# Kernel tuning notes

Hardware: AMD Instinct MI355X
Metric: run time of the kernel (lower is better)

## Reference

```python
import jax, jax.numpy as jnp
import numpy as np

N_NODES = 100000
N_EDGES = 1600000
FEAT_DIM = 64
IN_DIM = FEAT_DIM + 3  # feat + xyz


def setup_inputs() -> dict:
    key = jax.random.key(0)
    k1, k2, k3, k4, k5 = jax.random.split(key, 5)
    xyz = jax.random.normal(k1, (N_NODES, 3), dtype=jnp.float32)
    feat = jax.random.normal(k2, (N_NODES, FEAT_DIM), dtype=jnp.float32)
    edge_index = jax.random.randint(k3, (2, N_EDGES), 0, N_NODES, dtype=jnp.int64)
    # MLP params (Linear stored as [in, out] for x @ W + b)
    W1 = jax.random.normal(k4, (2 * IN_DIM, FEAT_DIM), dtype=jnp.float32) * (1.0 / np.sqrt(2 * IN_DIM))
    b1 = jnp.zeros((FEAT_DIM,), dtype=jnp.float32)
    W2 = jax.random.normal(k5, (FEAT_DIM, FEAT_DIM), dtype=jnp.float32) * (1.0 / np.sqrt(FEAT_DIM))
    b2 = jnp.zeros((FEAT_DIM,), dtype=jnp.float32)
    return {"xyz": xyz, "feat": feat, "edge_index": edge_index,
            "W1": W1, "b1": b1, "W2": W2, "b2": b2}


def reference(xyz, feat, edge_index, W1, b1, W2, b2):
    # node features: cat([feat, xyz]) -> [N, C+3]
    x = jnp.concatenate([feat, xyz], axis=-1)
    src = edge_index[0]  # j (source / neighbor)
    dst = edge_index[1]  # i (target, aggregation index)
    x_i = x[dst]                       # [E, C+3]
    x_j = x[src]                       # [E, C+3]
    # EdgeConv message: mlp(cat([x_i, x_j - x_i]))
    m = jnp.concatenate([x_i, x_j - x_i], axis=-1)   # [E, 2*(C+3)]
    h = jax.nn.relu(m @ W1 + b1) @ W2 + b2           # [E, C]
    n = x.shape[0]
    agg = jax.ops.segment_max(h, dst, num_segments=n)  # [N, C]
    # nodes with no incoming edges get 0 (matches PyG scatter-max fill)
    deg = jax.ops.segment_sum(jnp.ones((dst.shape[0],), h.dtype), dst, num_segments=n)
    return jnp.where(deg[:, None] > 0, agg, jnp.zeros_like(agg))
```

## Files before the change

kernel.cpp:

```cpp
#include <hip/hip_runtime.h>
#include <stdint.h>

#define N_NODES 100000
#define FEAT 64
#define NB 64
#define SC_CHUNK 8192
#define NBKT 1563
#define BKT_CAP 1400
#define RVN 6
#define BIAS 512.0f
#define NT_NODES 64
#define XT_STRIDE 68
#define SMEM_BYTES (67 * XT_STRIDE * 4 + 2 * 67 * 64 * 4)

typedef __attribute__((ext_vector_type(8))) _Float16 half8;
typedef __attribute__((ext_vector_type(2))) _Float16 half2v;
typedef __attribute__((ext_vector_type(2))) __fp16 fp16x2;
typedef __attribute__((ext_vector_type(4))) float f32x4;

__device__ __forceinline__ uint32_t enc_key(float f) {
    uint32_t u = __float_as_uint(f);
    return (u & 0x80000000u) ? ~u : (u | 0x80000000u);
}
__device__ __forceinline__ float dec_key(uint32_t k) {
    return __uint_as_float((k & 0x80000000u) ? (k & 0x7FFFFFFFu) : ~k);
}
__device__ __forceinline__ uint32_t pk_f16(float a, float b) {
    union { fp16x2 h; uint32_t u; } cv;
    cv.h = __builtin_amdgcn_cvt_pkrtz(a, b);
    return cv.u;
}

#define W2T_OFF 0
#define AMB_OFF 4096
#define BM_OFF  8384
#define W2P_OFF 12672
#define U_OFF   16384
#define V_OFF   (U_OFF + N_NODES * FEAT / 2)
#define GCNT_OFF (U_OFF + N_NODES * FEAT)
#define SRT_OFF  (GCNT_OFF + 2048)

__global__ __launch_bounds__(256) void transform_kernel(
    const float* __restrict__ W1, const float* __restrict__ W2,
    float* __restrict__ ws, int full)
{
    int i = blockIdx.x * 256 + threadIdx.x;
    if (i < 4096) {
        int c2 = i >> 6, c = i & 63;
        ws[W2T_OFF + i] = W2[c * 64 + c2];
    }
}

__global__ __launch_bounds__(256) void nodebkt_kernel(
    const float* __restrict__ xyz, const float* __restrict__ feat,
    const float* __restrict__ b1, const float* __restrict__ W1,
    const float* __restrict__ W2, float* __restrict__ ws,
    uint16_t* __restrict__ U, uint16_t* __restrict__ V, int nN,
    const int* __restrict__ ei, uint32_t* __restrict__ gcnt,
    uint32_t* __restrict__ sorted, int nE, int nBkt, int nodeBlocks)
{
    extern __shared__ float smem[];
    int t = threadIdx.x;

    if ((int)blockIdx.x < nBkt) {
        uint32_t* hist = (uint32_t*)smem;
        int e0 = blockIdx.x * SC_CHUNK;
        int cnt = min(SC_CHUNK, nE - e0);
        int cnt4 = cnt & ~3;

        for (int i = t; i < NBKT; i += 256) hist[i] = 0;
        __syncthreads();
        for (int i = t * 4; i < cnt4; i += 1024) {
            uint4 d4 = *(const uint4*)(ei + nE + e0 + i);
            atomicAdd(&hist[d4.x >> 6], 1u);
            atomicAdd(&hist[d4.y >> 6], 1u);
            atomicAdd(&hist[d4.z >> 6], 1u);
            atomicAdd(&hist[d4.w >> 6], 1u);
        }
        for (int i = cnt4 + t; i < cnt; i += 256)
            atomicAdd(&hist[ei[nE + e0 + i] >> 6], 1u);
        __syncthreads();
        for (int b = t; b < NBKT; b += 256) {
            uint32_t c = hist[b];
            hist[b] = c ? atomicAdd(&gcnt[b], c) : 0u;
        }
        __syncthreads();
        for (int i = t * 4; i < cnt4; i += 1024) {
            uint4 s4 = *(const uint4*)(ei + e0 + i);
            uint4 d4 = *(const uint4*)(ei + nE + e0 + i);
            uint32_t sa[4] = {(uint32_t)s4.x, (uint32_t)s4.y, (uint32_t)s4.z, (uint32_t)s4.w};
            uint32_t da[4] = {(uint32_t)d4.x, (uint32_t)d4.y, (uint32_t)d4.z, (uint32_t)d4.w};
            #pragma unroll
            for (int k = 0; k < 4; ++k) {
                uint32_t b = da[k] >> 6;
                uint32_t pos = atomicAdd(&hist[b], 1u);
                if (pos < BKT_CAP)
                    sorted[(size_t)b * BKT_CAP + pos] = sa[k] | ((da[k] & 63u) << 20);
            }
        }
        for (int i = cnt4 + t; i < cnt; i += 256) {
            uint32_t src = (uint32_t)ei[e0 + i];
            uint32_t dst = (uint32_t)ei[nE + e0 + i];
            uint32_t b = dst >> 6;
            uint32_t pos = atomicAdd(&hist[b], 1u);
            if (pos < BKT_CAP)
                sorted[(size_t)b * BKT_CAP + pos] = src | ((dst & 63u) << 20);
        }
        return;
    }

    int nb = (int)blockIdx.x - nBkt;
    if (nb >= nodeBlocks) {
        int p = (nb - nodeBlocks) * 256 + t;
        if (p < 4096) {
            int j = p & 7, c2lo = (p >> 3) & 15, quad = (p >> 7) & 3;
            int h = (p >> 9) & 1, n4 = (p >> 10) & 3;
            int k = h * 32 + quad * 8 + j;
            int n = n4 * 16 + c2lo;
            ((_Float16*)(ws + W2P_OFF))[p] = (_Float16)W2[k * 64 + n];
        }
        return;
    }

    float* xt = smem;
    float* wA = smem + 67 * XT_STRIDE;
    float* wB = wA + 67 * 64;

    int nb0 = nb * NT_NODES;
    int rows = min(NT_NODES, nN - nb0);

    for (int i4 = t; i4 < 67 * 16; i4 += 256) {
        float4 a = *(const float4*)(W1 + i4 * 4);
        float4 b = *(const float4*)(W1 + 67 * 64 + i4 * 4);
        float4 d;
        d.x = a.x - b.x; d.y = a.y - b.y; d.z = a.z - b.z; d.w = a.w - b.w;
        *(float4*)(wA + i4 * 4) = d;
        *(float4*)(wB + i4 * 4) = b;
    }
    for (int g4 = t; g4 < rows * 16; g4 += 256) {
        int row = g4 >> 4, c4 = (g4 & 15) * 4;
        float4 v = *(const float4*)(feat + (size_t)(nb0 + row) * FEAT + c4);
        xt[(c4 + 0) * XT_STRIDE + row] = v.x;
        xt[(c4 + 1) * XT_STRIDE + row] = v.y;
        xt[(c4 + 2) * XT_STRIDE + row] = v.z;
        xt[(c4 + 3) * XT_STRIDE + row] = v.w;
    }
    for (int i = t; i < 3 * NT_NODES; i += 256) {
        int k3 = i >> 6, row = i & 63;
        float v = (row < rows) ? xyz[(size_t)(nb0 + row) * 3 + k3] : 0.0f;
        xt[(64 + k3) * XT_STRIDE + row] = v;
    }
    __syncthreads();

    int cb = (t & 15) * 4;
    int ng = (t >> 4) * 4;

    float accU[4][4], accV[4][4];
    #pragma unroll
    for (int c = 0; c < 4; ++c) {
        float bv = b1[cb + c];
        #pragma unroll
        for (int r = 0; r < 4; ++r) { accU[r][c] = bv; accV[r][c] = 0.0f; }
    }

    const float* xrow = xt + ng;
    #pragma unroll 2
    for (int k = 0; k < 67; ++k) {
        float4 x0 = *(const float4*)(xrow + k * XT_STRIDE);
        float4 wa = *(const float4*)(wA + k * 64 + cb);
        float4 wb = *(const float4*)(wB + k * 64 + cb);
        float xv[4] = {x0.x, x0.y, x0.z, x0.w};
        float wav[4] = {wa.x, wa.y, wa.z, wa.w};
        float wbv[4] = {wb.x, wb.y, wb.z, wb.w};
        #pragma unroll
        for (int r = 0; r < 4; ++r) {
            #pragma unroll
            for (int c = 0; c < 4; ++c) {
                accU[r][c] = fmaf(xv[r], wav[c], accU[r][c]);
                accV[r][c] = fmaf(xv[r], wbv[c], accV[r][c]);
            }
        }
    }

    #pragma unroll
    for (int r = 0; r < 4; ++r) {
        if (ng + r < rows) {
            size_t n = (size_t)(nb0 + ng + r);
            uint2 oU; oU.x = pk_f16(accU[r][0], accU[r][1]);
                      oU.y = pk_f16(accU[r][2], accU[r][3]);
            *(uint2*)(U + n * FEAT + cb) = oU;
            uint2 oV; oV.x = pk_f16(accV[r][0], accV[r][1]);
                      oV.y = pk_f16(accV[r][2], accV[r][3]);
            *(uint2*)(V + n * FEAT + cb) = oV;
        }
    }
}

#define LOADE(G, DSV, VV0, VV1, UU0, UU1) do {                               \
        int e_c_ = min((G) + el, cnt - 1);                                   \
        uint32_t val_ = ssrt[e_c_];                                          \
        DSV = *(const uint4*)(ssrt + (G) + quad * 4);                        \
        int src_ = (int)(val_ & 0xFFFFFu);                                   \
        const uint32_t* vr_ = (const uint32_t*)(V + (size_t)src_ * FEAT);    \
        VV0 = *(const uint4*)(vr_ + quad * 4);                               \
        VV1 = *(const uint4*)(vr_ + 16 + quad * 4);                          \
        const uint32_t* ur_ = ushare + (int)(val_ >> 20) * 32;               \
        UU0 = *(const uint4*)(ur_ + quad * 4);                               \
        UU1 = *(const uint4*)(ur_ + 16 + quad * 4);                          \
    } while (0)

__global__ __launch_bounds__(256) void agg_kernel(
    const uint32_t* __restrict__ gcnt, const uint32_t* __restrict__ sorted,
    const uint16_t* __restrict__ U, const uint16_t* __restrict__ V,
    const float* __restrict__ ws_w2p, const float* __restrict__ b2,
    float* __restrict__ out, int nN)
{
    __shared__ int      lmax[NB * 65];
    __shared__ uint32_t ushare[NB * 32];
    __shared__ uint32_t ssrt[BKT_CAP + 16];
    __shared__ uint32_t shist[NB];

    int bkt = blockIdx.x;
    int nb0 = bkt * NB;
    int rows = min(NB, nN - nb0);
    int cnt = min((int)gcnt[bkt], BKT_CAP);
    int t = threadIdx.x;

    for (int i = t; i < NB * 65; i += 256) lmax[i] = 0;
    if (t < NB) shist[t] = 0;
    {
        const uint4* usrc4 = (const uint4*)(U + (size_t)nb0 * FEAT);
        for (int i = t; i < rows * 8; i += 256) ((uint4*)ushare)[i] = usrc4[i];
    }
    const uint32_t* bsrc = sorted + (size_t)bkt * BKT_CAP;
    __syncthreads();

    uint32_t rv[RVN];
    #pragma unroll
    for (int j = 0; j < RVN; ++j) {
        int i = t + j * 256;
        if (i < cnt) {
            uint32_t v = bsrc[i];
            rv[j] = v;
            atomicAdd(&shist[v >> 20], 1u);
        }
    }
    __syncthreads();
    if (t < NB) {
        uint32_t v = shist[t];
        uint32_t run = v;
        #pragma unroll
        for (int d = 1; d < 64; d <<= 1) {
            uint32_t x = (uint32_t)__shfl_up((int)run, (unsigned)d, 64);
            if (t >= d) run += x;
        }
        shist[t] = run - v;
    }
    __syncthreads();
    #pragma unroll
    for (int j = 0; j < RVN; ++j) {
        int i = t + j * 256;
        if (i < cnt) {
            uint32_t v = rv[j];
            uint32_t pos = atomicAdd(&shist[v >> 20], 1u);
            ssrt[pos] = v;
        }
    }
    __syncthreads();

    int lane = t & 63;
    int wave = t >> 6;
    int el = lane & 15, quad = lane >> 4;

    const uint4* w2p = (const uint4*)ws_w2p;
    union { uint4 u4; half8 h8; } bfr[8];
    #pragma unroll
    for (int q8 = 0; q8 < 8; ++q8)
        bfr[q8].u4 = w2p[(q8 * 4 + quad) * 16 + el];
    float b2v[4];
    #pragma unroll
    for (int n4 = 0; n4 < 4; ++n4) b2v[n4] = b2[n4 * 16 + el] + BIAS;

    const half2v zero2 = {(_Float16)0.0f, (_Float16)0.0f};

    uint4 dsv_c, vv_c0, vv_c1, uu_c0, uu_c1;
    int g = wave * 16;
    if (g < cnt) LOADE(g, dsv_c, vv_c0, vv_c1, uu_c0, uu_c1);

    #pragma unroll 1
    for (; g < cnt; g += 64) {
        int gn = g + 64;
        int gl = (gn < cnt) ? gn : g;
        uint4 dsv_n, vv_n0, vv_n1, uu_n0, uu_n1;
        LOADE(gl, dsv_n, vv_n0, vv_n1, uu_n0, uu_n1);

        union { uint4 u4; half8 h8; } afr[2];
        #pragma unroll
        for (int h = 0; h < 2; ++h) {
            uint4 uu = h ? uu_c1 : uu_c0;
            uint4 vv = h ? vv_c1 : vv_c0;
            uint32_t ua[4] = {uu.x, uu.y, uu.z, uu.w};
            uint32_t va[4] = {vv.x, vv.y, vv.z, vv.w};
            uint32_t pk[4];
            #pragma unroll
            for (int p = 0; p < 4; ++p) {
                union { uint32_t u; half2v h2; } cu, cv2, ct;
                cu.u = ua[p]; cv2.u = va[p];
                ct.h2 = __builtin_elementwise_max(cu.h2 + cv2.h2, zero2);
                pk[p] = ct.u;
            }
            afr[h].u4 = make_uint4(pk[0], pk[1], pk[2], pk[3]);
        }

        f32x4 acc[4];
        #pragma unroll
        for (int n4 = 0; n4 < 4; ++n4)
            acc[n4] = (f32x4){b2v[n4], b2v[n4], b2v[n4], b2v[n4]};
        #pragma unroll
        for (int n4 = 0; n4 < 4; ++n4) {
            acc[n4] = __builtin_amdgcn_mfma_f32_16x16x32_f16(afr[0].h8, bfr[n4*2+0].h8, acc[n4], 0, 0, 0);
            acc[n4] = __builtin_amdgcn_mfma_f32_16x16x32_f16(afr[1].h8, bfr[n4*2+1].h8, acc[n4], 0, 0, 0);
        }

        int d0 = (int)(dsv_c.x >> 20), d1 = (int)(dsv_c.y >> 20);
        int d2 = (int)(dsv_c.z >> 20), d3 = (int)(dsv_c.w >> 20);
        int eb = g + quad * 4;
        bool ok0 = eb < cnt, ok1 = eb + 1 < cnt;
        bool ok2 = eb + 2 < cnt, ok3 = eb + 3 < cnt;
        bool m0 = (d0 == d1) & ok1;
        bool m1 = (d1 == d2) & ok2;
        bool m2 = (d2 == d3) & ok3;
        #pragma unroll
        for (int n4 = 0; n4 < 4; ++n4) {
            if (m0) acc[n4][1] = fmaxf(acc[n4][1], acc[n4][0]);
            if (m1) acc[n4][2] = fmaxf(acc[n4][2], acc[n4][1]);
            if (m2) acc[n4][3] = fmaxf(acc[n4][3], acc[n4][2]);
        }
        if (ok0 & !m0) {
            #pragma unroll
            for (int n4 = 0; n4 < 4; ++n4)
                atomicMax(&lmax[d0 * 65 + n4 * 16 + el], __float_as_int(acc[n4][0]));
        }
        if (ok1 & !m1) {
            #pragma unroll
            for (int n4 = 0; n4 < 4; ++n4)
                atomicMax(&lmax[d1 * 65 + n4 * 16 + el], __float_as_int(acc[n4][1]));
        }
        if (ok2 & !m2) {
            #pragma unroll
            for (int n4 = 0; n4 < 4; ++n4)
                atomicMax(&lmax[d2 * 65 + n4 * 16 + el], __float_as_int(acc[n4][2]));
        }
        if (ok3) {
            #pragma unroll
            for (int n4 = 0; n4 < 4; ++n4)
                atomicMax(&lmax[d3 * 65 + n4 * 16 + el], __float_as_int(acc[n4][3]));
        }

        dsv_c = dsv_n;
        vv_c0 = vv_n0; vv_c1 = vv_n1;
        uu_c0 = uu_n0; uu_c1 = uu_n1;
    }
    __syncthreads();

    for (int i = t * 4; i < rows * FEAT; i += 1024) {
        int r = i >> 6, c = i & 63;
        int lb = r * 65 + c;
        int k0 = lmax[lb + 0], k1 = lmax[lb + 1];
        int k2 = lmax[lb + 2], k3 = lmax[lb + 3];
        float4 o;
        o.x = k0 ? (__int_as_float(k0) - BIAS) : 0.0f;
        o.y = k1 ? (__int_as_float(k1) - BIAS) : 0.0f;
        o.z = k2 ? (__int_as_float(k2) - BIAS) : 0.0f;
        o.w = k3 ? (__int_as_float(k3) - BIAS) : 0.0f;
        *(float4*)(out + (size_t)(nb0 + r) * FEAT + c) = o;
    }
}
#undef LOADE

__device__ __forceinline__ void rank1_update(
    float* __restrict__ h, float xi, float d,
    const float* __restrict__ A, const float* __restrict__ B)
{
    #pragma unroll
    for (int c = 0; c < FEAT; ++c)
        h[c] = fmaf(xi, A[c], fmaf(d, B[c], h[c]));
}

__global__ __launch_bounds__(256) void edge_fused_kernel(
    const float* __restrict__ xyz, const float* __restrict__ feat,
    const int* __restrict__ ei,
    const float* __restrict__ W1, const float* __restrict__ b1,
    const float* __restrict__ ws, const float* __restrict__ b2,
    uint32_t* __restrict__ keys, int nE)
{
    int e = blockIdx.x * 256 + threadIdx.x;
    if (e >= nE) return;
    int src = ei[e];
    int dst = ei[nE + e];
    const float* __restrict__ W2T = ws + W2T_OFF;

    float h[FEAT];
    #pragma unroll
    for (int c = 0; c < FEAT; ++c) h[c] = b1[c];

    const float* fi = feat + (size_t)dst * FEAT;
    const float* fj = feat + (size_t)src * FEAT;
    #pragma unroll 1
    for (int k = 0; k < 64; k += 4) {
        float4 a = *(const float4*)(fi + k);
        float4 b = *(const float4*)(fj + k);
        rank1_update(h, a.x, b.x - a.x, W1 + (k + 0) * 64, W1 + (67 + k + 0) * 64);
        rank1_update(h, a.y, b.y - a.y, W1 + (k + 1) * 64, W1 + (67 + k + 1) * 64);
        rank1_update(h, a.z, b.z - a.z, W1 + (k + 2) * 64, W1 + (67 + k + 2) * 64);
        rank1_update(h, a.w, b.w - a.w, W1 + (k + 3) * 64, W1 + (67 + k + 3) * 64);
    }
    {
        const float* pi = xyz + (size_t)dst * 3;
        const float* pj = xyz + (size_t)src * 3;
        #pragma unroll
        for (int k3 = 0; k3 < 3; ++k3) {
            float xi = pi[k3];
            rank1_update(h, xi, pj[k3] - xi, W1 + (64 + k3) * 64, W1 + (131 + k3) * 64);
        }
    }
    #pragma unroll
    for (int c = 0; c < FEAT; ++c) h[c] = fmaxf(h[c], 0.0f);

    uint32_t* krow = keys + (size_t)dst * FEAT;
    #pragma unroll 1
    for (int c2 = 0; c2 < FEAT; c2 += 4) {
        float o0 = b2[c2 + 0], o1 = b2[c2 + 1];
        float o2 = b2[c2 + 2], o3 = b2[c2 + 3];
        const float* w0 = W2T + (c2 + 0) * 64;
        const float* w1 = W2T + (c2 + 1) * 64;
        const float* w2 = W2T + (c2 + 2) * 64;
        const float* w3 = W2T + (c2 + 3) * 64;
        #pragma unroll
        for (int c = 0; c < FEAT; ++c) {
            float hv = h[c];
            o0 = fmaf(hv, w0[c], o0);
            o1 = fmaf(hv, w1[c], o1);
            o2 = fmaf(hv, w2[c], o2);
            o3 = fmaf(hv, w3[c], o3);
        }
        uint32_t k0 = enc_key(o0), k1 = enc_key(o1);
        uint32_t k2 = enc_key(o2), k3 = enc_key(o3);
        uint4 cur = *(const uint4*)(krow + c2);
        if (k0 > cur.x) atomicMax(&krow[c2 + 0], k0);
        if (k1 > cur.y) atomicMax(&krow[c2 + 1], k1);
        if (k2 > cur.z) atomicMax(&krow[c2 + 2], k2);
        if (k3 > cur.w) atomicMax(&krow[c2 + 3], k3);
    }
}

__global__ __launch_bounds__(256) void decode_kernel(
    uint32_t* __restrict__ keys, int n4)
{
    int i = blockIdx.x * 256 + threadIdx.x;
    if (i >= n4) return;
    uint4 k = ((const uint4*)keys)[i];
    float4 r;
    r.x = k.x ? dec_key(k.x) : 0.0f;
    r.y = k.y ? dec_key(k.y) : 0.0f;
    r.z = k.z ? dec_key(k.z) : 0.0f;
    r.w = k.w ? dec_key(k.w) : 0.0f;
    ((float4*)keys)[i] = r;
}

extern "C" void kernel_launch(void* const* d_in, const int* in_sizes, int n_in,
                              void* d_out, int out_size, void* d_ws, size_t ws_size,
                              hipStream_t stream)
{
    const float* xyz  = (const float*)d_in[0];
    const float* feat = (const float*)d_in[1];
    const int*   ei   = (const int*)d_in[2];
    const float* W1   = (const float*)d_in[3];
    const float* b1   = (const float*)d_in[4];
    const float* W2   = (const float*)d_in[5];
    const float* b2   = (const float*)d_in[6];

    int nE = in_sizes[2] / 2;
    float* ws = (float*)d_ws;

    size_t need_words = (size_t)SRT_OFF + (size_t)NBKT * BKT_CAP;
    int full = (ws_size >= need_words * 4) ? 1 : 0;

    if (full) {
        uint16_t* U = (uint16_t*)(ws + U_OFF);
        uint16_t* V = (uint16_t*)(ws + V_OFF);
        uint32_t* gcnt   = (uint32_t*)(ws + GCNT_OFF);
        uint32_t* sorted = (uint32_t*)(ws + SRT_OFF);

        hipMemsetAsync(gcnt, 0, NBKT * sizeof(uint32_t), stream);
        int nBkt = (nE + SC_CHUNK - 1) / SC_CHUNK;
        int nodeBlocks = (N_NODES + NT_NODES - 1) / NT_NODES;
        int packBlocks = 16;
        nodebkt_kernel<<<nBkt + nodeBlocks + packBlocks, 256, SMEM_BYTES, stream>>>(
            xyz, feat, b1, W1, W2, ws, U, V, N_NODES, ei, gcnt, sorted, nE,
            nBkt, nodeBlocks);
        agg_kernel<<<NBKT, 256, 0, stream>>>(
            gcnt, sorted, U, V, ws + W2P_OFF, b2, (float*)d_out, N_NODES);
    } else {
        uint32_t* keys = (uint32_t*)d_out;
        transform_kernel<<<16, 256, 0, stream>>>(W1, W2, ws, 0);
        hipMemsetAsync(d_out, 0, (size_t)out_size * sizeof(float), stream);
        edge_fused_kernel<<<(nE + 255) / 256, 256, 0, stream>>>(
            xyz, feat, ei, W1, b1, ws, b2, keys, nE);
        decode_kernel<<<(out_size / 4 + 255) / 256, 256, 0, stream>>>(
            keys, out_size / 4);
    }
}
```

Before: 173.5 us.

## Fold edge bucketing into node blocks via global atomics; pad shared U rows

Removes the separate bucket-scatter blocks, which built a shared-memory histogram and reserved ranges per chunk. Instead, each node-transform block scatters a 1024-edge slice directly using one global atomicAdd per edge on the bucket counters, overlapping bucketing with the node GEMM work. The shared U tile in the aggregation kernel is also padded to a 36-word row stride to reduce LDS bank conflicts. The trade is roughly 1.6M global atomics on about 1563 counters, which may contend heavily, in place of cheap LDS atomics plus a few global ones. The edge coverage of 1563 blocks times 1024 edges just covers the 1.6M edges.

```diff
diff --git a/kernel.cpp b/kernel.cpp
--- a/kernel.cpp
+++ b/kernel.cpp
@@ -4,13 +4,14 @@
 #define N_NODES 100000
 #define FEAT 64
 #define NB 64
-#define SC_CHUNK 8192
 #define NBKT 1563
 #define BKT_CAP 1400
 #define RVN 6
 #define BIAS 512.0f
 #define NT_NODES 64
 #define XT_STRIDE 68
+#define EDGE_SLICE 1024
+#define USTRIDE 36
 #define SMEM_BYTES (67 * XT_STRIDE * 4 + 2 * 67 * 64 * 4)
 
 typedef __attribute__((ext_vector_type(8))) _Float16 half8;
@@ -57,59 +58,12 @@
     const float* __restrict__ W2, float* __restrict__ ws,
     uint16_t* __restrict__ U, uint16_t* __restrict__ V, int nN,
     const int* __restrict__ ei, uint32_t* __restrict__ gcnt,
-    uint32_t* __restrict__ sorted, int nE, int nBkt, int nodeBlocks)
+    uint32_t* __restrict__ sorted, int nE, int nodeBlocks)
 {
     extern __shared__ float smem[];
     int t = threadIdx.x;
-
-    if ((int)blockIdx.x < nBkt) {
-        uint32_t* hist = (uint32_t*)smem;
-        int e0 = blockIdx.x * SC_CHUNK;
-        int cnt = min(SC_CHUNK, nE - e0);
-        int cnt4 = cnt & ~3;
-
-        for (int i = t; i < NBKT; i += 256) hist[i] = 0;
-        __syncthreads();
-        for (int i = t * 4; i < cnt4; i += 1024) {
-            uint4 d4 = *(const uint4*)(ei + nE + e0 + i);
-            atomicAdd(&hist[d4.x >> 6], 1u);
-            atomicAdd(&hist[d4.y >> 6], 1u);
-            atomicAdd(&hist[d4.z >> 6], 1u);
-            atomicAdd(&hist[d4.w >> 6], 1u);
-        }
-        for (int i = cnt4 + t; i < cnt; i += 256)
-            atomicAdd(&hist[ei[nE + e0 + i] >> 6], 1u);
-        __syncthreads();
-        for (int b = t; b < NBKT; b += 256) {
-            uint32_t c = hist[b];
-            hist[b] = c ? atomicAdd(&gcnt[b], c) : 0u;
-        }
-        __syncthreads();
-        for (int i = t * 4; i < cnt4; i += 1024) {
-            uint4 s4 = *(const uint4*)(ei + e0 + i);
-            uint4 d4 = *(const uint4*)(ei + nE + e0 + i);
-            uint32_t sa[4] = {(uint32_t)s4.x, (uint32_t)s4.y, (uint32_t)s4.z, (uint32_t)s4.w};
-            uint32_t da[4] = {(uint32_t)d4.x, (uint32_t)d4.y, (uint32_t)d4.z, (uint32_t)d4.w};
-            #pragma unroll
-            for (int k = 0; k < 4; ++k) {
-                uint32_t b = da[k] >> 6;
-                uint32_t pos = atomicAdd(&hist[b], 1u);
-                if (pos < BKT_CAP)
-                    sorted[(size_t)b * BKT_CAP + pos] = sa[k] | ((da[k] & 63u) << 20);
-            }
-        }
-        for (int i = cnt4 + t; i < cnt; i += 256) {
-            uint32_t src = (uint32_t)ei[e0 + i];
-            uint32_t dst = (uint32_t)ei[nE + e0 + i];
-            uint32_t b = dst >> 6;
-            uint32_t pos = atomicAdd(&hist[b], 1u);
-            if (pos < BKT_CAP)
-                sorted[(size_t)b * BKT_CAP + pos] = src | ((dst & 63u) << 20);
-        }
-        return;
-    }
-
-    int nb = (int)blockIdx.x - nBkt;
+    int nb = (int)blockIdx.x;
+
     if (nb >= nodeBlocks) {
         int p = (nb - nodeBlocks) * 256 + t;
         if (p < 4096) {
@@ -149,6 +103,33 @@
         int k3 = i >> 6, row = i & 63;
         float v = (row < rows) ? xyz[(size_t)(nb0 + row) * 3 + k3] : 0.0f;
         xt[(64 + k3) * XT_STRIDE + row] = v;
+    }
+
+    {
+        int e0 = nb * EDGE_SLICE;
+        int ecnt = min(EDGE_SLICE, nE - e0);
+        int ecnt4 = ecnt & ~3;
+        for (int i = t * 4; i < ecnt4; i += 1024) {
+            uint4 s4 = *(const uint4*)(ei + e0 + i);
+            uint4 d4 = *(const uint4*)(ei + nE + e0 + i);
+            uint32_t sa[4] = {(uint32_t)s4.x, (uint32_t)s4.y, (uint32_t)s4.z, (uint32_t)s4.w};
+            uint32_t da[4] = {(uint32_t)d4.x, (uint32_t)d4.y, (uint32_t)d4.z, (uint32_t)d4.w};
+            #pragma unroll
+            for (int k = 0; k < 4; ++k) {
+                uint32_t b = da[k] >> 6;
+                uint32_t pos = atomicAdd(&gcnt[b], 1u);
+                if (pos < BKT_CAP)
+                    sorted[(size_t)b * BKT_CAP + pos] = sa[k] | ((da[k] & 63u) << 20);
+            }
+        }
+        for (int i = ecnt4 + t; i < ecnt; i += 256) {
+            uint32_t src = (uint32_t)ei[e0 + i];
+            uint32_t dst = (uint32_t)ei[nE + e0 + i];
+            uint32_t b = dst >> 6;
+            uint32_t pos = atomicAdd(&gcnt[b], 1u);
+            if (pos < BKT_CAP)
+                sorted[(size_t)b * BKT_CAP + pos] = src | ((dst & 63u) << 20);
+        }
     }
     __syncthreads();
 
@@ -204,7 +185,7 @@
         const uint32_t* vr_ = (const uint32_t*)(V + (size_t)src_ * FEAT);    \
         VV0 = *(const uint4*)(vr_ + quad * 4);                               \
         VV1 = *(const uint4*)(vr_ + 16 + quad * 4);                          \
-        const uint32_t* ur_ = ushare + (int)(val_ >> 20) * 32;               \
+        const uint32_t* ur_ = ushare + (int)(val_ >> 20) * USTRIDE;          \
         UU0 = *(const uint4*)(ur_ + quad * 4);                               \
         UU1 = *(const uint4*)(ur_ + 16 + quad * 4);                          \
     } while (0)
@@ -216,7 +197,7 @@
     float* __restrict__ out, int nN)
 {
     __shared__ int      lmax[NB * 65];
-    __shared__ uint32_t ushare[NB * 32];
+    __shared__ uint32_t ushare[NB * USTRIDE];
     __shared__ uint32_t ssrt[BKT_CAP + 16];
     __shared__ uint32_t shist[NB];
 
@@ -230,7 +211,10 @@
     if (t < NB) shist[t] = 0;
     {
         const uint4* usrc4 = (const uint4*)(U + (size_t)nb0 * FEAT);
-        for (int i = t; i < rows * 8; i += 256) ((uint4*)ushare)[i] = usrc4[i];
+        for (int i = t; i < rows * 8; i += 256) {
+            int row = i >> 3, q = i & 7;
+            *(uint4*)(ushare + row * USTRIDE + q * 4) = usrc4[i];
+        }
     }
     const uint32_t* bsrc = sorted + (size_t)bkt * BKT_CAP;
     __syncthreads();
@@ -493,12 +477,11 @@
         uint32_t* sorted = (uint32_t*)(ws + SRT_OFF);
 
         hipMemsetAsync(gcnt, 0, NBKT * sizeof(uint32_t), stream);
-        int nBkt = (nE + SC_CHUNK - 1) / SC_CHUNK;
         int nodeBlocks = (N_NODES + NT_NODES - 1) / NT_NODES;
         int packBlocks = 16;
-        nodebkt_kernel<<<nBkt + nodeBlocks + packBlocks, 256, SMEM_BYTES, stream>>>(
+        nodebkt_kernel<<<nodeBlocks + packBlocks, 256, SMEM_BYTES, stream>>>(
             xyz, feat, b1, W1, W2, ws, U, V, N_NODES, ei, gcnt, sorted, nE,
-            nBkt, nodeBlocks);
+            nodeBlocks);
         agg_kernel<<<NBKT, 256, 0, stream>>>(
             gcnt, sorted, U, V, ws + W2P_OFF, b2, (float*)d_out, N_NODES);
     } else {
```

New measurement: 380.9 us. 2.2x slower.
